# Kernel optimization log

Hardware: AMD Instinct MI355X
Metric: run time of the kernel (lower is better)

The kernel has to match this reference:

```python
import jax, jax.numpy as jnp
import numpy as np

B, S, D = 64, 500, 1024  # batch, seq_len, input_dim == hidden_dim
MAX_POS = 500

def _lin(k, din, dout):
    k1, k2 = jax.random.split(k)
    s = 1.0 / np.sqrt(din)
    W = jax.random.uniform(k1, (din, dout), jnp.float32, -s, s)
    b = jax.random.uniform(k2, (dout,), jnp.float32, -s, s)
    return W, b

def setup_inputs() -> dict:
    key = jax.random.key(0)
    ks = jax.random.split(key, 12)
    x = jax.random.normal(ks[0], (B, S, D), jnp.float32)
    pos_emb = jax.random.normal(ks[1], (MAX_POS, D), jnp.float32)
    Wq_fw, bq_fw = _lin(ks[2], D, D)
    Wk_fw, bk_fw = _lin(ks[3], D, D)
    Wv_fw, bv_fw = _lin(ks[4], D, D)
    Wq_bw, bq_bw = _lin(ks[5], D, D)
    Wk_bw, bk_bw = _lin(ks[6], D, D)
    Wv_bw, bv_bw = _lin(ks[7], D, D)
    Wg_fw, bg_fw = _lin(ks[8], 2 * D, D)
    Wg_bw, bg_bw = _lin(ks[9], 2 * D, D)
    W2, b2 = _lin(ks[10], 2 * D, 2 * D)
    W1, b1 = _lin(ks[11], 2 * D, 2 * D)
    return dict(x=x, pos_emb=pos_emb,
                Wq_fw=Wq_fw, bq_fw=bq_fw, Wk_fw=Wk_fw, bk_fw=bk_fw, Wv_fw=Wv_fw, bv_fw=bv_fw,
                Wq_bw=Wq_bw, bq_bw=bq_bw, Wk_bw=Wk_bw, bk_bw=bk_bw, Wv_bw=Wv_bw, bv_bw=bv_bw,
                Wg_fw=Wg_fw, bg_fw=bg_fw, Wg_bw=Wg_bw, bg_bw=bg_bw,
                W2=W2, b2=b2, W1=W1, b1=b1)

def _attn(q, k, v, mask, d):
    # q,k,v: [B,S,D]; mask: [S,S] bool (True = keep)
    scores = jnp.einsum('bqd,bkd->bqk', q, k) / jnp.sqrt(jnp.float32(d))
    scores = jnp.where(mask[None], scores, jnp.float32(-1e9))
    probs = jax.nn.softmax(scores, axis=-1)  # dropout is identity in eval
    return jnp.einsum('bqk,bkd->bqd', probs, v)

def reference(x, pos_emb, Wq_fw, bq_fw, Wk_fw, bk_fw, Wv_fw, bv_fw,
              Wq_bw, bq_bw, Wk_bw, bk_bw, Wv_bw, bv_bw,
              Wg_fw, bg_fw, Wg_bw, bg_bw, W2, b2, W1, b1):
    b, s, d = x.shape
    H = x + pos_emb[:s][None]  # [B,S,D]
    tri = jnp.tril(jnp.ones((s, s), dtype=bool))
    H_mF = _attn(H @ Wq_fw + bq_fw, H @ Wk_fw + bk_fw, H @ Wv_fw + bv_fw, tri, d)
    H_mB = _attn(H @ Wq_bw + bq_bw, H @ Wk_bw + bk_bw, H @ Wv_bw + bv_bw, tri.T, d)
    G_fw = jax.nn.sigmoid(jnp.concatenate([H, H_mF], -1) @ Wg_fw + bg_fw)
    C_F = G_fw * H + (1.0 - G_fw) * H_mF
    G_bw = jax.nn.sigmoid(jnp.concatenate([H, H_mB], -1) @ Wg_bw + bg_bw)
    C_B = G_bw * H + (1.0 - G_bw) * H_mB
    C_i = jnp.concatenate([C_F, C_B], -1)  # [B,S,2D]
    activ = jax.nn.sigmoid(C_i @ W2 + b2)
    scores = activ @ W1 + b1
    attn_w = jax.nn.softmax(scores, axis=1)  # softmax over seq dim
    utt_vec = jnp.sum(attn_w * C_i, axis=1)  # [B,2D]
    return utt_vec, C_i
```

## Files before the change

kernel.cpp:

```cpp
#include <hip/hip_runtime.h>

typedef __bf16 bf16;
typedef __bf16 bf16x4 __attribute__((ext_vector_type(4)));
typedef __bf16 bf16x8 __attribute__((ext_vector_type(8)));
typedef float  f32x4  __attribute__((ext_vector_type(4)));
typedef unsigned int u32;

#define GLD_LDS16(gsrc, ldst) \
  __builtin_amdgcn_global_load_lds((const __attribute__((address_space(1))) u32*)(gsrc), \
                                   (__attribute__((address_space(3))) u32*)(ldst), 16, 0, 0)

static __device__ __forceinline__ float sigmoidf_(float x) { return 1.0f / (1.0f + expf(-x)); }

__global__ void fill_guard(float* __restrict__ utt, float v) {
  int i = blockIdx.x * 256 + threadIdx.x;
  if (i < 131072) utt[i] = v;
}

__global__ void add_pos_bf(const float* __restrict__ x, const float* __restrict__ pos,
                           bf16* __restrict__ H) {
  size_t i = ((size_t)blockIdx.x * 256 + threadIdx.x) * 4;
  if (i >= 32768000ull) return;
  int d = (int)(i & 1023);
  int s = (int)((i >> 10) % 500);
  float4 xv = *(const float4*)(x + i);
  float4 pv = *(const float4*)(pos + (size_t)s * 1024 + d);
  bf16x4 o;
  o[0] = (bf16)(xv.x + pv.x); o[1] = (bf16)(xv.y + pv.y);
  o[2] = (bf16)(xv.z + pv.z); o[3] = (bf16)(xv.w + pv.w);
  *(bf16x4*)(H + i) = o;
}

__global__ void wtrans(const float* __restrict__ src, bf16* __restrict__ dst, int R, int C) {
  __shared__ float tile[32][33];
  int c0 = blockIdx.x * 32, r0 = blockIdx.y * 32;
  int tr = threadIdx.x >> 5, tc = threadIdx.x & 31;
#pragma unroll
  for (int i = 0; i < 4; ++i)
    tile[tr + i * 8][tc] = src[(size_t)(r0 + tr + i * 8) * C + c0 + tc];
  __syncthreads();
#pragma unroll
  for (int i = 0; i < 4; ++i) {
    int rr = tr + i * 8;
    dst[(size_t)(c0 + rr) * R + r0 + tc] = (bf16)tile[tc][rr];
  }
}

template <int EPI, typename TC>
__global__ __launch_bounds__(256, 2) void mgemm(
    const bf16* __restrict__ A, const bf16* __restrict__ A2, int ksplit,
    const bf16* __restrict__ Bt, const float* __restrict__ bias, TC* __restrict__ C,
    bf16* __restrict__ Cbf,
    int M, int N, int K, int lda, int ldb, int ldc, int c_off, float scale,
    long long sA, long long sB, long long sC,
    const bf16* __restrict__ Gh, const bf16* __restrict__ Gm) {
  __shared__ __align__(16) char sm[16384];
  const int t = threadIdx.x;
  const long long bz = blockIdx.z;
  A += bz * sA; A2 += bz * sA; Bt += bz * sB; C += bz * sC;

  const int gx = gridDim.x;
  const int nwg = gx * gridDim.y;
  const int orig = blockIdx.y * gx + blockIdx.x;
  const int qq = nwg >> 3, r8 = nwg & 7;
  const int xcd = orig & 7, lo = orig >> 3;
  const int wg = (xcd < r8 ? xcd * (qq + 1) : r8 * (qq + 1) + (xcd - r8) * qq) + lo;
  const int m0 = (wg / gx) * 128, n0 = (wg % gx) * 128;

  f32x4 acc[4][4];
#pragma unroll
  for (int i = 0; i < 4; ++i)
#pragma unroll
    for (int j = 0; j < 4; ++j)
#pragma unroll
      for (int c = 0; c < 4; ++c) acc[i][j][c] = 0.0f;

  const int lane = t & 63;
  const int wv = t >> 6, wm = (wv >> 1) * 64, wn = (wv & 1) * 64;
  const int lr = lane & 15, lkb = (lane >> 4) * 16;
  const int rr = t >> 2, cc = (t & 3) * 8;

  for (int k0 = 0; k0 < K; k0 += 32) {
    const bf16* Ak = (k0 < ksplit) ? (A + k0) : (A2 + (k0 - ksplit));
    const bf16* Bk = Bt + k0;
#pragma unroll
    for (int j = 0; j < 2; ++j) {
      int ra = m0 + j * 64 + rr; ra = ra < M ? ra : M - 1;
      GLD_LDS16(Ak + (size_t)ra * lda + cc, sm + j * 4096 + t * 16);
      int rb = n0 + j * 64 + rr; rb = rb < N ? rb : N - 1;
      GLD_LDS16(Bk + (size_t)rb * ldb + cc, sm + 8192 + j * 4096 + t * 16);
    }
    asm volatile("s_waitcnt vmcnt(0)" ::: "memory");
    __syncthreads();

    bf16x8 av[4], bv[4];
#pragma unroll
    for (int i = 0; i < 4; ++i) {
      av[i] = *(const bf16x8*)(sm + (wm + i * 16 + lr) * 64 + lkb);
      bv[i] = *(const bf16x8*)(sm + 8192 + (wn + i * 16 + lr) * 64 + lkb);
    }
#pragma unroll
    for (int i = 0; i < 4; ++i)
#pragma unroll
      for (int j = 0; j < 4; ++j)
        acc[i][j] = __builtin_amdgcn_mfma_f32_16x16x32_bf16(av[i], bv[j], acc[i][j], 0, 0, 0);
    __syncthreads();
  }

#pragma unroll
  for (int i = 0; i < 4; ++i) {
#pragma unroll
    for (int j4 = 0; j4 < 4; ++j4) {
      int m = m0 + wm + i * 16 + (lane >> 4) * 4 + j4;
      if (m >= M) continue;
#pragma unroll
      for (int j = 0; j < 4; ++j) {
        int n = n0 + wn + j * 16 + (lane & 15);
        if (n >= N) continue;
        float v = acc[i][j][j4] * scale;
        if (bias) v += bias[n];
        if (EPI == 1) v = sigmoidf_(v);
        if (EPI == 2) {
          float g = sigmoidf_(v);
          float h  = (float)Gh[(size_t)m * 1024 + n];
          float hm = (float)Gm[(size_t)m * 1024 + n];
          v = g * h + (1.0f - g) * hm;
        }
        if (EPI == 3) {
          unsigned b = (unsigned)m / 500u;
          unsigned s = (unsigned)m - b * 500u;
          C[(size_t)b * 524288 + (size_t)n * 512 + s] = (TC)v;
        } else {
          C[(size_t)m * ldc + c_off + n] = (TC)v;
          if (EPI == 2 && Cbf) Cbf[(size_t)m * 2048 + c_off + n] = (bf16)v;
        }
      }
    }
  }
}

__global__ void attn_softmax_w(const float* __restrict__ S, bf16* __restrict__ P, int fw) {
  int row = blockIdx.x * 4 + (threadIdx.x >> 6);
  int lane = threadIdx.x & 63;
  int q = row % 500;
  const float* Srow = S + (size_t)row * 512;
  bf16* Prow = P + (size_t)row * 512;
  int klo = fw ? 0 : q;
  int khi = fw ? q : 499;

  float xv[8];
  float m = -1e30f;
#pragma unroll
  for (int i = 0; i < 8; ++i) {
    int k = lane + i * 64;
    bool valid = (k >= klo) & (k <= khi);
    float v = valid ? Srow[k] : -1e30f;
    xv[i] = v;
    m = fmaxf(m, v);
  }
#pragma unroll
  for (int off = 32; off > 0; off >>= 1) m = fmaxf(m, __shfl_xor(m, off, 64));
  float e[8];
  float sum = 0.0f;
#pragma unroll
  for (int i = 0; i < 8; ++i) {
    e[i] = (xv[i] > -1e29f) ? expf(xv[i] - m) : 0.0f;
    sum += e[i];
  }
#pragma unroll
  for (int off = 32; off > 0; off >>= 1) sum += __shfl_xor(sum, off, 64);
  float inv = 1.0f / sum;
#pragma unroll
  for (int i = 0; i < 8; ++i) Prow[lane + i * 64] = (bf16)(e[i] * inv);
}

__global__ void final_reduce_chunk(const float* __restrict__ s2, const float* __restrict__ Ci,
                                   float* __restrict__ utt) {
  int c = blockIdx.x * 256 + threadIdx.x;
  int b = blockIdx.y;
  if (c >= 2048) return;
  float m = -1e30f, sum = 0.0f, acc = 0.0f;
  for (int s = 0; s < 500; ++s) {
    size_t idx = ((size_t)(b * 500 + s)) * 2048 + c;
    float xx = s2[idx];
    float ci = Ci[idx];
    float mn = fmaxf(m, xx);
    float corr = expf(m - mn);
    float e = expf(xx - mn);
    sum = sum * corr + e;
    acc = acc * corr + e * ci;
    m = mn;
  }
  utt[(size_t)b * 2048 + c] = acc / sum;
}

extern "C" void kernel_launch(void* const* d_in, const int* in_sizes, int n_in,
                              void* d_out, int out_size, void* d_ws, size_t ws_size,
                              hipStream_t stream) {
  (void)in_sizes; (void)n_in; (void)out_size;
  float* utt = (float*)d_out;
  float* Ci  = (float*)d_out + 131072;

  const float* x     = (const float*)d_in[0];
  const float* pos   = (const float*)d_in[1];
  const float* Wq_fw = (const float*)d_in[2];  const float* bq_fw = (const float*)d_in[3];
  const float* Wk_fw = (const float*)d_in[4];  const float* bk_fw = (const float*)d_in[5];
  const float* Wv_fw = (const float*)d_in[6];  const float* bv_fw = (const float*)d_in[7];
  const float* Wq_bw = (const float*)d_in[8];  const float* bq_bw = (const float*)d_in[9];
  const float* Wk_bw = (const float*)d_in[10]; const float* bk_bw = (const float*)d_in[11];
  const float* Wv_bw = (const float*)d_in[12]; const float* bv_bw = (const float*)d_in[13];
  const float* Wg_fw = (const float*)d_in[14]; const float* bg_fw = (const float*)d_in[15];
  const float* Wg_bw = (const float*)d_in[16]; const float* bg_bw = (const float*)d_in[17];
  const float* W2    = (const float*)d_in[18]; const float* b2    = (const float*)d_in[19];
  const float* W1    = (const float*)d_in[20]; const float* b1    = (const float*)d_in[21];

  const size_t WS_BYTES = 465305600ull;
  if (ws_size < WS_BYTES) { fill_guard<<<512, 256, 0, stream>>>(utt, 500.0f); return; }

  char* wsb = (char*)d_ws;
  bf16*  Hbf  = (bf16*)(wsb);
  bf16*  Qb   = (bf16*)(wsb + 65536000);
  bf16*  Kb   = (bf16*)(wsb + 131072000);
  bf16*  Vt   = (bf16*)(wsb + 196608000);
  float* Sb   = (float*)(wsb + 263716864);
  bf16*  Hmb  = (bf16*)(wsb + 263716864);
  bf16*  Pb   = (bf16*)(wsb + 329252864);
  char*  wts  = wsb + 362020864;
  bf16* WqF = (bf16*)(wts);             bf16* WkF = (bf16*)(wts + 2097152);
  bf16* WvF = (bf16*)(wts + 4194304);   bf16* WqB = (bf16*)(wts + 6291456);
  bf16* WkB = (bf16*)(wts + 8388608);   bf16* WvB = (bf16*)(wts + 10485760);
  bf16* WgF = (bf16*)(wts + 12582912);  bf16* WgB = (bf16*)(wts + 16777216);
  bf16* W2t = (bf16*)(wts + 20971520);  bf16* W1t = (bf16*)(wts + 29360128);
  bf16*  Cibf  = (bf16*)(wsb + 399769600);
  bf16*  activ = (bf16*)(wsb + 131072000);
  float* s2b   = (float*)(wsb);

  add_pos_bf<<<32000, 256, 0, stream>>>(x, pos, Hbf);

  struct WT { const float* s; bf16* d; int R, C; } wt[10] = {
      {Wq_fw, WqF, 1024, 1024}, {Wk_fw, WkF, 1024, 1024}, {Wv_fw, WvF, 1024, 1024},
      {Wq_bw, WqB, 1024, 1024}, {Wk_bw, WkB, 1024, 1024}, {Wv_bw, WvB, 1024, 1024},
      {Wg_fw, WgF, 2048, 1024}, {Wg_bw, WgB, 2048, 1024},
      {W2,    W2t, 2048, 2048}, {W1,    W1t, 2048, 2048}};
  for (int i = 0; i < 10; ++i)
    wtrans<<<dim3(wt[i].C / 32, wt[i].R / 32), 256, 0, stream>>>(wt[i].s, wt[i].d, wt[i].R, wt[i].C);

  const int BIG = 1 << 30;
  for (int dir = 0; dir < 2; ++dir) {
    const bf16* WqT = dir ? WqB : WqF;  const float* bq = dir ? bq_bw : bq_fw;
    const bf16* WkT = dir ? WkB : WkF;  const float* bk = dir ? bk_bw : bk_fw;
    const bf16* WvT = dir ? WvB : WvF;  const float* bv = dir ? bv_bw : bv_fw;
    const bf16* WgT = dir ? WgB : WgF;  const float* bg = dir ? bg_bw : bg_fw;

    mgemm<0, bf16><<<dim3(8, 250, 1), 256, 0, stream>>>(
        Hbf, Hbf, BIG, WqT, bq, Qb, nullptr, 32000, 1024, 1024, 1024, 1024, 1024, 0, 1.0f,
        0, 0, 0, nullptr, nullptr);
    mgemm<0, bf16><<<dim3(8, 250, 1), 256, 0, stream>>>(
        Hbf, Hbf, BIG, WkT, bk, Kb, nullptr, 32000, 1024, 1024, 1024, 1024, 1024, 0, 1.0f,
        0, 0, 0, nullptr, nullptr);
    mgemm<3, bf16><<<dim3(8, 250, 1), 256, 0, stream>>>(
        Hbf, Hbf, BIG, WvT, bv, Vt, nullptr, 32000, 1024, 1024, 1024, 1024, 512, 0, 1.0f,
        0, 0, 0, nullptr, nullptr);
    mgemm<0, float><<<dim3(4, 4, 64), 256, 0, stream>>>(
        Qb, Qb, BIG, Kb, nullptr, Sb, nullptr, 500, 500, 1024, 1024, 1024, 512, 0, 0.03125f,
        512000, 512000, 256000, nullptr, nullptr);
    attn_softmax_w<<<8000, 256, 0, stream>>>(Sb, Pb, dir == 0 ? 1 : 0);
    mgemm<0, bf16><<<dim3(8, 4, 64), 256, 0, stream>>>(
        Pb, Pb, BIG, Vt, nullptr, Hmb, nullptr, 500, 1024, 512, 512, 512, 1024, 0, 1.0f,
        256000, 524288, 512000, nullptr, nullptr);
    mgemm<2, float><<<dim3(8, 250, 1), 256, 0, stream>>>(
        Hbf, Hmb, 1024, WgT, bg, Ci, Cibf, 32000, 1024, 2048, 1024, 2048, 2048,
        dir == 0 ? 0 : 1024, 1.0f, 0, 0, 0, Hbf, Hmb);
  }

  mgemm<1, bf16><<<dim3(16, 250, 1), 256, 0, stream>>>(
      Cibf, Cibf, BIG, W2t, b2, activ, nullptr, 32000, 2048, 2048, 2048, 2048, 2048, 0, 1.0f,
      0, 0, 0, nullptr, nullptr);

  for (int c0 = 0; c0 < 2; ++c0) {
    mgemm<0, float><<<dim3(16, 125, 1), 256, 0, stream>>>(
        activ + (size_t)c0 * 16000 * 2048, activ, BIG, W1t, b1, s2b, nullptr,
        16000, 2048, 2048, 2048, 2048, 2048, 0, 1.0f, 0, 0, 0, nullptr, nullptr);
    final_reduce_chunk<<<dim3(8, 32), 256, 0, stream>>>(
        s2b, Ci + (size_t)c0 * 32 * 500 * 2048, utt + (size_t)c0 * 32 * 2048);
  }
}
```

Measured before the change: 2.610 ms.

## Add 256x256 double-buffered swizzled GEMM kernel for large projection GEMMs

Adds a new 512-thread GEMM kernel with 256x256 output tiles, K-step 64, double-buffered LDS (128KB dynamic shared memory) with XOR-swizzled layout, and prefetch of the next tile interleaved with MFMA phases using setprio. The large dense projections (Q/K/V, gates, W2, W1) switch to it, while the batched attention GEMMs keep the old 128x128 kernel, now stripped of the unused Cbf argument and XCD remapping. The aim is more data reuse per load and overlap of global loads with compute. The cost is much higher register and LDS use, which leaves only one block per CU.

```diff
diff --git a/kernel.cpp b/kernel.cpp
--- a/kernel.cpp
+++ b/kernel.cpp
@@ -47,17 +47,14 @@
 }
 
 template <int EPI, typename TC>
-__global__ __launch_bounds__(256, 2) void mgemm(
+__global__ __launch_bounds__(512, 2) void mgemm256(
     const bf16* __restrict__ A, const bf16* __restrict__ A2, int ksplit,
     const bf16* __restrict__ Bt, const float* __restrict__ bias, TC* __restrict__ C,
     bf16* __restrict__ Cbf,
     int M, int N, int K, int lda, int ldb, int ldc, int c_off, float scale,
-    long long sA, long long sB, long long sC,
     const bf16* __restrict__ Gh, const bf16* __restrict__ Gm) {
-  __shared__ __align__(16) char sm[16384];
+  extern __shared__ char sm[];
   const int t = threadIdx.x;
-  const long long bz = blockIdx.z;
-  A += bz * sA; A2 += bz * sA; Bt += bz * sB; C += bz * sC;
 
   const int gx = gridDim.x;
   const int nwg = gx * gridDim.y;
@@ -65,59 +62,107 @@
   const int qq = nwg >> 3, r8 = nwg & 7;
   const int xcd = orig & 7, lo = orig >> 3;
   const int wg = (xcd < r8 ? xcd * (qq + 1) : r8 * (qq + 1) + (xcd - r8) * qq) + lo;
-  const int m0 = (wg / gx) * 128, n0 = (wg % gx) * 128;
-
-  f32x4 acc[4][4];
-#pragma unroll
-  for (int i = 0; i < 4; ++i)
+  const int m0 = (wg / gx) * 256, n0 = (wg % gx) * 256;
+
+  const int lane = t & 63;
+  const int w = t >> 6, wr = w >> 2, wc = w & 3;
+  const int srow = t >> 3, schunk = t & 7, scol = schunk * 8;
+  const int hi16 = (lane >> 4) << 4;
+
+  f32x4 acc[8][4];
+#pragma unroll
+  for (int i = 0; i < 8; ++i)
 #pragma unroll
     for (int j = 0; j < 4; ++j)
 #pragma unroll
       for (int c = 0; c < 4; ++c) acc[i][j][c] = 0.0f;
 
-  const int lane = t & 63;
-  const int wv = t >> 6, wm = (wv >> 1) * 64, wn = (wv & 1) * 64;
-  const int lr = lane & 15, lkb = (lane >> 4) * 16;
-  const int rr = t >> 2, cc = (t & 3) * 8;
-
-  for (int k0 = 0; k0 < K; k0 += 32) {
-    const bf16* Ak = (k0 < ksplit) ? (A + k0) : (A2 + (k0 - ksplit));
-    const bf16* Bk = Bt + k0;
-#pragma unroll
-    for (int j = 0; j < 2; ++j) {
-      int ra = m0 + j * 64 + rr; ra = ra < M ? ra : M - 1;
-      GLD_LDS16(Ak + (size_t)ra * lda + cc, sm + j * 4096 + t * 16);
-      int rb = n0 + j * 64 + rr; rb = rb < N ? rb : N - 1;
-      GLD_LDS16(Bk + (size_t)rb * ldb + cc, sm + 8192 + j * 4096 + t * 16);
-    }
-    asm volatile("s_waitcnt vmcnt(0)" ::: "memory");
-    __syncthreads();
-
-    bf16x8 av[4], bv[4];
-#pragma unroll
-    for (int i = 0; i < 4; ++i) {
-      av[i] = *(const bf16x8*)(sm + (wm + i * 16 + lr) * 64 + lkb);
-      bv[i] = *(const bf16x8*)(sm + 8192 + (wn + i * 16 + lr) * 64 + lkb);
-    }
-#pragma unroll
-    for (int i = 0; i < 4; ++i)
-#pragma unroll
-      for (int j = 0; j < 4; ++j)
-        acc[i][j] = __builtin_amdgcn_mfma_f32_16x16x32_bf16(av[i], bv[j], acc[i][j], 0, 0, 0);
-    __syncthreads();
-  }
-
-#pragma unroll
-  for (int i = 0; i < 4; ++i) {
+#define STAGE_Q(tt, cb, h) do {                                                     \
+    const int k0s_ = (tt) * 64;                                                     \
+    char* lb_ = sm + (cb) * 65536 + ((h) < 2 ? 0 : 32768);                          \
+    _Pragma("unroll")                                                               \
+    for (int i_ = 0; i_ < 2; ++i_) {                                                \
+      int rl_ = ((h) & 1) * 128 + i_ * 64 + srow;                                   \
+      int cx_ = scol ^ ((rl_ & 7) << 3);                                            \
+      if ((h) < 2) {                                                                \
+        int rg_ = m0 + rl_; rg_ = rg_ < M ? rg_ : M - 1;                            \
+        const bf16* s_ = (k0s_ < ksplit)                                            \
+            ? A  + (size_t)rg_ * lda + k0s_ + cx_                                   \
+            : A2 + (size_t)rg_ * lda + (k0s_ - ksplit) + cx_;                       \
+        GLD_LDS16(s_, lb_ + rl_ * 128 + schunk * 16);                               \
+      } else {                                                                      \
+        int rg_ = n0 + rl_; rg_ = rg_ < N ? rg_ : N - 1;                            \
+        GLD_LDS16(Bt + (size_t)rg_ * ldb + k0s_ + cx_, lb_ + rl_ * 128 + schunk * 16); \
+      }                                                                             \
+    }                                                                               \
+  } while (0)
+
+  const int NT = K >> 6;
+  STAGE_Q(0, 0, 0); STAGE_Q(0, 0, 1); STAGE_Q(0, 0, 2); STAGE_Q(0, 0, 3);
+
+  for (int t0 = 0; t0 < NT; ++t0) {
+    const int cur = t0 & 1;
+    char* smA = sm + cur * 65536;
+    char* smB = smA + 32768;
+    const bool pf = (t0 + 1 < NT);
+
+    if (pf) {
+      STAGE_Q(t0 + 1, cur ^ 1, 0);
+      asm volatile("s_waitcnt vmcnt(2)" ::: "memory");
+    } else {
+      asm volatile("s_waitcnt vmcnt(0)" ::: "memory");
+    }
+    __builtin_amdgcn_s_barrier();
+
+    bf16x8 bfr[4][2];
+#pragma unroll
+    for (int fc = 0; fc < 4; ++fc)
+#pragma unroll
+      for (int ks = 0; ks < 2; ++ks) {
+        int rb = wc * 64 + fc * 16 + (lane & 15);
+        int byb = (ks * 64 + hi16) ^ ((rb & 7) << 4);
+        bfr[fc][ks] = *(const bf16x8*)(smB + rb * 128 + byb);
+      }
+
+#pragma unroll
+    for (int p = 0; p < 4; ++p) {
+      if (p > 0 && pf) STAGE_Q(t0 + 1, cur ^ 1, p);
+      bf16x8 afr[2][2];
+#pragma unroll
+      for (int e = 0; e < 2; ++e)
+#pragma unroll
+        for (int ks = 0; ks < 2; ++ks) {
+          int ra = wr * 128 + (2 * p + e) * 16 + (lane & 15);
+          int bya = (ks * 64 + hi16) ^ ((ra & 7) << 4);
+          afr[e][ks] = *(const bf16x8*)(smA + ra * 128 + bya);
+        }
+      if (p > 0) __builtin_amdgcn_s_barrier();
+      __builtin_amdgcn_s_setprio(1);
+#pragma unroll
+      for (int e = 0; e < 2; ++e)
+#pragma unroll
+        for (int fc = 0; fc < 4; ++fc)
+#pragma unroll
+          for (int ks = 0; ks < 2; ++ks)
+            acc[2 * p + e][fc] = __builtin_amdgcn_mfma_f32_16x16x32_bf16(
+                afr[e][ks], bfr[fc][ks], acc[2 * p + e][fc], 0, 0, 0);
+      __builtin_amdgcn_s_setprio(0);
+      __builtin_amdgcn_s_barrier();
+    }
+  }
+#undef STAGE_Q
+
+#pragma unroll
+  for (int fr = 0; fr < 8; ++fr) {
 #pragma unroll
     for (int j4 = 0; j4 < 4; ++j4) {
-      int m = m0 + wm + i * 16 + (lane >> 4) * 4 + j4;
+      int m = m0 + wr * 128 + fr * 16 + ((lane >> 4) << 2) + j4;
       if (m >= M) continue;
 #pragma unroll
-      for (int j = 0; j < 4; ++j) {
-        int n = n0 + wn + j * 16 + (lane & 15);
+      for (int fc = 0; fc < 4; ++fc) {
+        int n = n0 + wc * 64 + fc * 16 + (lane & 15);
         if (n >= N) continue;
-        float v = acc[i][j][j4] * scale;
+        float v = acc[fr][fc][j4] * scale;
         if (bias) v += bias[n];
         if (EPI == 1) v = sigmoidf_(v);
         if (EPI == 2) {
@@ -139,6 +184,77 @@
   }
 }
 
+template <int EPI, typename TC>
+__global__ __launch_bounds__(256, 2) void mgemm(
+    const bf16* __restrict__ A, const bf16* __restrict__ A2, int ksplit,
+    const bf16* __restrict__ Bt, const float* __restrict__ bias, TC* __restrict__ C,
+    int M, int N, int K, int lda, int ldb, int ldc, int c_off, float scale,
+    long long sA, long long sB, long long sC,
+    const bf16* __restrict__ Gh, const bf16* __restrict__ Gm) {
+  __shared__ __align__(16) char sm[16384];
+  const int t = threadIdx.x;
+  const long long bz = blockIdx.z;
+  A += bz * sA; A2 += bz * sA; Bt += bz * sB; C += bz * sC;
+  const int m0 = blockIdx.y * 128, n0 = blockIdx.x * 128;
+
+  f32x4 acc[4][4];
+#pragma unroll
+  for (int i = 0; i < 4; ++i)
+#pragma unroll
+    for (int j = 0; j < 4; ++j)
+#pragma unroll
+      for (int c = 0; c < 4; ++c) acc[i][j][c] = 0.0f;
+
+  const int lane = t & 63;
+  const int wv = t >> 6, wm = (wv >> 1) * 64, wn = (wv & 1) * 64;
+  const int lr = lane & 15, lkb = (lane >> 4) * 16;
+  const int rr = t >> 2, cc = (t & 3) * 8;
+
+  for (int k0 = 0; k0 < K; k0 += 32) {
+    const bf16* Ak = (k0 < ksplit) ? (A + k0) : (A2 + (k0 - ksplit));
+    const bf16* Bk = Bt + k0;
+#pragma unroll
+    for (int j = 0; j < 2; ++j) {
+      int ra = m0 + j * 64 + rr; ra = ra < M ? ra : M - 1;
+      GLD_LDS16(Ak + (size_t)ra * lda + cc, sm + j * 4096 + t * 16);
+      int rb = n0 + j * 64 + rr; rb = rb < N ? rb : N - 1;
+      GLD_LDS16(Bk + (size_t)rb * ldb + cc, sm + 8192 + j * 4096 + t * 16);
+    }
+    asm volatile("s_waitcnt vmcnt(0)" ::: "memory");
+    __syncthreads();
+
+    bf16x8 av[4], bv[4];
+#pragma unroll
+    for (int i = 0; i < 4; ++i) {
+      av[i] = *(const bf16x8*)(sm + (wm + i * 16 + lr) * 64 + lkb);
+      bv[i] = *(const bf16x8*)(sm + 8192 + (wn + i * 16 + lr) * 64 + lkb);
+    }
+#pragma unroll
+    for (int i = 0; i < 4; ++i)
+#pragma unroll
+      for (int j = 0; j < 4; ++j)
+        acc[i][j] = __builtin_amdgcn_mfma_f32_16x16x32_bf16(av[i], bv[j], acc[i][j], 0, 0, 0);
+    __syncthreads();
+  }
+
+#pragma unroll
+  for (int i = 0; i < 4; ++i) {
+#pragma unroll
+    for (int j4 = 0; j4 < 4; ++j4) {
+      int m = m0 + wm + i * 16 + (lane >> 4) * 4 + j4;
+      if (m >= M) continue;
+#pragma unroll
+      for (int j = 0; j < 4; ++j) {
+        int n = n0 + wn + j * 16 + (lane & 15);
+        if (n >= N) continue;
+        float v = acc[i][j][j4] * scale;
+        if (bias) v += bias[n];
+        C[(size_t)m * ldc + c_off + n] = (TC)v;
+      }
+    }
+  }
+}
+
 __global__ void attn_softmax_w(const float* __restrict__ S, bf16* __restrict__ P, int fw) {
   int row = blockIdx.x * 4 + (threadIdx.x >> 6);
   int lane = threadIdx.x & 63;
@@ -235,6 +351,17 @@
   bf16*  activ = (bf16*)(wsb + 131072000);
   float* s2b   = (float*)(wsb);
 
+  hipFuncSetAttribute(reinterpret_cast<const void*>(&mgemm256<0, bf16>),
+                      hipFuncAttributeMaxDynamicSharedMemorySize, 131072);
+  hipFuncSetAttribute(reinterpret_cast<const void*>(&mgemm256<3, bf16>),
+                      hipFuncAttributeMaxDynamicSharedMemorySize, 131072);
+  hipFuncSetAttribute(reinterpret_cast<const void*>(&mgemm256<2, float>),
+                      hipFuncAttributeMaxDynamicSharedMemorySize, 131072);
+  hipFuncSetAttribute(reinterpret_cast<const void*>(&mgemm256<1, bf16>),
+                      hipFuncAttributeMaxDynamicSharedMemorySize, 131072);
+  hipFuncSetAttribute(reinterpret_cast<const void*>(&mgemm256<0, float>),
+                      hipFuncAttributeMaxDynamicSharedMemorySize, 131072);
+
   add_pos_bf<<<32000, 256, 0, stream>>>(x, pos, Hbf);
 
   struct WT { const float* s; bf16* d; int R, C; } wt[10] = {
@@ -252,35 +379,35 @@
     const bf16* WvT = dir ? WvB : WvF;  const float* bv = dir ? bv_bw : bv_fw;
     const bf16* WgT = dir ? WgB : WgF;  const float* bg = dir ? bg_bw : bg_fw;
 
-    mgemm<0, bf16><<<dim3(8, 250, 1), 256, 0, stream>>>(
+    mgemm256<0, bf16><<<dim3(4, 125), 512, 131072, stream>>>(
         Hbf, Hbf, BIG, WqT, bq, Qb, nullptr, 32000, 1024, 1024, 1024, 1024, 1024, 0, 1.0f,
-        0, 0, 0, nullptr, nullptr);
-    mgemm<0, bf16><<<dim3(8, 250, 1), 256, 0, stream>>>(
+        nullptr, nullptr);
+    mgemm256<0, bf16><<<dim3(4, 125), 512, 131072, stream>>>(
         Hbf, Hbf, BIG, WkT, bk, Kb, nullptr, 32000, 1024, 1024, 1024, 1024, 1024, 0, 1.0f,
-        0, 0, 0, nullptr, nullptr);
-    mgemm<3, bf16><<<dim3(8, 250, 1), 256, 0, stream>>>(
+        nullptr, nullptr);
+    mgemm256<3, bf16><<<dim3(4, 125), 512, 131072, stream>>>(
         Hbf, Hbf, BIG, WvT, bv, Vt, nullptr, 32000, 1024, 1024, 1024, 1024, 512, 0, 1.0f,
-        0, 0, 0, nullptr, nullptr);
+        nullptr, nullptr);
     mgemm<0, float><<<dim3(4, 4, 64), 256, 0, stream>>>(
-        Qb, Qb, BIG, Kb, nullptr, Sb, nullptr, 500, 500, 1024, 1024, 1024, 512, 0, 0.03125f,
+        Qb, Qb, BIG, Kb, nullptr, Sb, 500, 500, 1024, 1024, 1024, 512, 0, 0.03125f,
         512000, 512000, 256000, nullptr, nullptr);
     attn_softmax_w<<<8000, 256, 0, stream>>>(Sb, Pb, dir == 0 ? 1 : 0);
     mgemm<0, bf16><<<dim3(8, 4, 64), 256, 0, stream>>>(
-        Pb, Pb, BIG, Vt, nullptr, Hmb, nullptr, 500, 1024, 512, 512, 512, 1024, 0, 1.0f,
+        Pb, Pb, BIG, Vt, nullptr, Hmb, 500, 1024, 512, 512, 512, 1024, 0, 1.0f,
         256000, 524288, 512000, nullptr, nullptr);
-    mgemm<2, float><<<dim3(8, 250, 1), 256, 0, stream>>>(
+    mgemm256<2, float><<<dim3(8, 125), 512, 131072, stream>>>(
         Hbf, Hmb, 1024, WgT, bg, Ci, Cibf, 32000, 1024, 2048, 1024, 2048, 2048,
-        dir == 0 ? 0 : 1024, 1.0f, 0, 0, 0, Hbf, Hmb);
-  }
-
-  mgemm<1, bf16><<<dim3(16, 250, 1), 256, 0, stream>>>(
+        dir == 0 ? 0 : 1024, 1.0f, Hbf, Hmb);
+  }
+
+  mgemm256<1, bf16><<<dim3(8, 125), 512, 131072, stream>>>(
       Cibf, Cibf, BIG, W2t, b2, activ, nullptr, 32000, 2048, 2048, 2048, 2048, 2048, 0, 1.0f,
-      0, 0, 0, nullptr, nullptr);
+      nullptr, nullptr);
 
   for (int c0 = 0; c0 < 2; ++c0) {
-    mgemm<0, float><<<dim3(16, 125, 1), 256, 0, stream>>>(
+    mgemm256<0, float><<<dim3(8, 63), 512, 131072, stream>>>(
         activ + (size_t)c0 * 16000 * 2048, activ, BIG, W1t, b1, s2b, nullptr,
-        16000, 2048, 2048, 2048, 2048, 2048, 0, 1.0f, 0, 0, 0, nullptr, nullptr);
+        16000, 2048, 2048, 2048, 2048, 2048, 0, 1.0f, nullptr, nullptr);
     final_reduce_chunk<<<dim3(8, 32), 256, 0, stream>>>(
         s2b, Ci + (size_t)c0 * 32 * 500 * 2048, utt + (size_t)c0 * 32 * 2048);
   }
```

Result: slower. 2.856 ms (+9.4%).

## Fuse QKV projections into one GEMM and use K=64 tiles with XOR-swizzled LDS

Applied to the files above, without the earlier changes.

The Q, K and V projections now run as a single GEMM with N=3072 over the contiguous transposed weights. A new epilogue routes each column range to Q, K or the transposed V layout, each with its own bias. The GEMM main loop now stages 64-wide K slices into a 32KB LDS buffer with an XOR swizzle, to halve barrier and loop overhead and to avoid LDS bank conflicts. The larger LDS footprint may lower occupancy, and the fused epilogue adds branching.

```diff
diff --git a/kernel.cpp b/kernel.cpp
--- a/kernel.cpp
+++ b/kernel.cpp
@@ -49,12 +49,13 @@
 template <int EPI, typename TC>
 __global__ __launch_bounds__(256, 2) void mgemm(
     const bf16* __restrict__ A, const bf16* __restrict__ A2, int ksplit,
-    const bf16* __restrict__ Bt, const float* __restrict__ bias, TC* __restrict__ C,
-    bf16* __restrict__ Cbf,
+    const bf16* __restrict__ Bt, const float* __restrict__ bias,
+    const float* __restrict__ biasK, const float* __restrict__ biasV,
+    TC* __restrict__ C, bf16* __restrict__ Cbf, bf16* __restrict__ Cv,
     int M, int N, int K, int lda, int ldb, int ldc, int c_off, float scale,
     long long sA, long long sB, long long sC,
     const bf16* __restrict__ Gh, const bf16* __restrict__ Gm) {
-  __shared__ __align__(16) char sm[16384];
+  __shared__ __align__(16) char sm[32768];
   const int t = threadIdx.x;
   const long long bz = blockIdx.z;
   A += bz * sA; A2 += bz * sA; Bt += bz * sB; C += bz * sC;
@@ -77,33 +78,44 @@
 
   const int lane = t & 63;
   const int wv = t >> 6, wm = (wv >> 1) * 64, wn = (wv & 1) * 64;
-  const int lr = lane & 15, lkb = (lane >> 4) * 16;
-  const int rr = t >> 2, cc = (t & 3) * 8;
-
-  for (int k0 = 0; k0 < K; k0 += 32) {
+  const int lr = lane & 15, lhi = lane >> 4;
+  const int srow8 = t >> 3, sch = t & 7;
+
+  for (int k0 = 0; k0 < K; k0 += 64) {
     const bf16* Ak = (k0 < ksplit) ? (A + k0) : (A2 + (k0 - ksplit));
     const bf16* Bk = Bt + k0;
 #pragma unroll
-    for (int j = 0; j < 2; ++j) {
-      int ra = m0 + j * 64 + rr; ra = ra < M ? ra : M - 1;
-      GLD_LDS16(Ak + (size_t)ra * lda + cc, sm + j * 4096 + t * 16);
-      int rb = n0 + j * 64 + rr; rb = rb < N ? rb : N - 1;
-      GLD_LDS16(Bk + (size_t)rb * ldb + cc, sm + 8192 + j * 4096 + t * 16);
+    for (int i = 0; i < 4; ++i) {
+      int rl = i * 32 + srow8;
+      int ra = m0 + rl; ra = ra < M ? ra : M - 1;
+      int ca = (sch ^ (ra & 7)) * 8;
+      GLD_LDS16(Ak + (size_t)ra * lda + ca, sm + rl * 128 + sch * 16);
+      int rb = n0 + rl; rb = rb < N ? rb : N - 1;
+      int cb = (sch ^ (rb & 7)) * 8;
+      GLD_LDS16(Bk + (size_t)rb * ldb + cb, sm + 16384 + rl * 128 + sch * 16);
     }
     asm volatile("s_waitcnt vmcnt(0)" ::: "memory");
     __syncthreads();
 
-    bf16x8 av[4], bv[4];
-#pragma unroll
-    for (int i = 0; i < 4; ++i) {
-      av[i] = *(const bf16x8*)(sm + (wm + i * 16 + lr) * 64 + lkb);
-      bv[i] = *(const bf16x8*)(sm + 8192 + (wn + i * 16 + lr) * 64 + lkb);
-    }
+    bf16x8 av[4][2], bv[4][2];
 #pragma unroll
     for (int i = 0; i < 4; ++i)
 #pragma unroll
-      for (int j = 0; j < 4; ++j)
-        acc[i][j] = __builtin_amdgcn_mfma_f32_16x16x32_bf16(av[i], bv[j], acc[i][j], 0, 0, 0);
+      for (int ks = 0; ks < 2; ++ks) {
+        int ra = wm + i * 16 + lr;
+        int ga = ks * 4 + lhi;
+        av[i][ks] = *(const bf16x8*)(sm + ra * 128 + ((ga ^ (ra & 7)) << 4));
+        int rb = wn + i * 16 + lr;
+        bv[i][ks] = *(const bf16x8*)(sm + 16384 + rb * 128 + ((ga ^ (rb & 7)) << 4));
+      }
+#pragma unroll
+    for (int ks = 0; ks < 2; ++ks)
+#pragma unroll
+      for (int i = 0; i < 4; ++i)
+#pragma unroll
+        for (int j = 0; j < 4; ++j)
+          acc[i][j] = __builtin_amdgcn_mfma_f32_16x16x32_bf16(av[i][ks], bv[j][ks],
+                                                              acc[i][j], 0, 0, 0);
     __syncthreads();
   }
 
@@ -111,13 +123,23 @@
   for (int i = 0; i < 4; ++i) {
 #pragma unroll
     for (int j4 = 0; j4 < 4; ++j4) {
-      int m = m0 + wm + i * 16 + (lane >> 4) * 4 + j4;
+      int m = m0 + wm + i * 16 + lhi * 4 + j4;
       if (m >= M) continue;
 #pragma unroll
       for (int j = 0; j < 4; ++j) {
-        int n = n0 + wn + j * 16 + (lane & 15);
+        int n = n0 + wn + j * 16 + lr;
         if (n >= N) continue;
         float v = acc[i][j][j4] * scale;
+        if (EPI == 4) {
+          const float* bp = (n < 1024) ? bias : (n < 2048) ? biasK : biasV;
+          v += bp[n & 1023];
+          unsigned b = (unsigned)m / 500u;
+          unsigned s = (unsigned)m - b * 500u;
+          if (n < 1024)       C  [(size_t)m * 1024 + n] = (TC)v;
+          else if (n < 2048)  Cbf[(size_t)m * 1024 + (n - 1024)] = (bf16)v;
+          else                Cv [(size_t)b * 524288 + (size_t)(n - 2048) * 512 + s] = (bf16)v;
+          continue;
+        }
         if (bias) v += bias[n];
         if (EPI == 1) v = sigmoidf_(v);
         if (EPI == 2) {
@@ -126,14 +148,8 @@
           float hm = (float)Gm[(size_t)m * 1024 + n];
           v = g * h + (1.0f - g) * hm;
         }
-        if (EPI == 3) {
-          unsigned b = (unsigned)m / 500u;
-          unsigned s = (unsigned)m - b * 500u;
-          C[(size_t)b * 524288 + (size_t)n * 512 + s] = (TC)v;
-        } else {
-          C[(size_t)m * ldc + c_off + n] = (TC)v;
-          if (EPI == 2 && Cbf) Cbf[(size_t)m * 2048 + c_off + n] = (bf16)v;
-        }
+        C[(size_t)m * ldc + c_off + n] = (TC)v;
+        if (EPI == 2 && Cbf) Cbf[(size_t)m * 2048 + c_off + n] = (bf16)v;
       }
     }
   }
@@ -226,9 +242,8 @@
   bf16*  Hmb  = (bf16*)(wsb + 263716864);
   bf16*  Pb   = (bf16*)(wsb + 329252864);
   char*  wts  = wsb + 362020864;
-  bf16* WqF = (bf16*)(wts);             bf16* WkF = (bf16*)(wts + 2097152);
-  bf16* WvF = (bf16*)(wts + 4194304);   bf16* WqB = (bf16*)(wts + 6291456);
-  bf16* WkB = (bf16*)(wts + 8388608);   bf16* WvB = (bf16*)(wts + 10485760);
+  bf16* WqF = (bf16*)(wts);
+  bf16* WqB = (bf16*)(wts + 6291456);
   bf16* WgF = (bf16*)(wts + 12582912);  bf16* WgB = (bf16*)(wts + 16777216);
   bf16* W2t = (bf16*)(wts + 20971520);  bf16* W1t = (bf16*)(wts + 29360128);
   bf16*  Cibf  = (bf16*)(wsb + 399769600);
@@ -238,8 +253,9 @@
   add_pos_bf<<<32000, 256, 0, stream>>>(x, pos, Hbf);
 
   struct WT { const float* s; bf16* d; int R, C; } wt[10] = {
-      {Wq_fw, WqF, 1024, 1024}, {Wk_fw, WkF, 1024, 1024}, {Wv_fw, WvF, 1024, 1024},
-      {Wq_bw, WqB, 1024, 1024}, {Wk_bw, WkB, 1024, 1024}, {Wv_bw, WvB, 1024, 1024},
+      {Wq_fw, WqF, 1024, 1024}, {Wk_fw, (bf16*)(wts + 2097152), 1024, 1024},
+      {Wv_fw, (bf16*)(wts + 4194304), 1024, 1024}, {Wq_bw, WqB, 1024, 1024},
+      {Wk_bw, (bf16*)(wts + 8388608), 1024, 1024}, {Wv_bw, (bf16*)(wts + 10485760), 1024, 1024},
       {Wg_fw, WgF, 2048, 1024}, {Wg_bw, WgB, 2048, 1024},
       {W2,    W2t, 2048, 2048}, {W1,    W1t, 2048, 2048}};
   for (int i = 0; i < 10; ++i)
@@ -247,40 +263,40 @@
 
   const int BIG = 1 << 30;
   for (int dir = 0; dir < 2; ++dir) {
-    const bf16* WqT = dir ? WqB : WqF;  const float* bq = dir ? bq_bw : bq_fw;
-    const bf16* WkT = dir ? WkB : WkF;  const float* bk = dir ? bk_bw : bk_fw;
-    const bf16* WvT = dir ? WvB : WvF;  const float* bv = dir ? bv_bw : bv_fw;
-    const bf16* WgT = dir ? WgB : WgF;  const float* bg = dir ? bg_bw : bg_fw;
-
-    mgemm<0, bf16><<<dim3(8, 250, 1), 256, 0, stream>>>(
-        Hbf, Hbf, BIG, WqT, bq, Qb, nullptr, 32000, 1024, 1024, 1024, 1024, 1024, 0, 1.0f,
-        0, 0, 0, nullptr, nullptr);
-    mgemm<0, bf16><<<dim3(8, 250, 1), 256, 0, stream>>>(
-        Hbf, Hbf, BIG, WkT, bk, Kb, nullptr, 32000, 1024, 1024, 1024, 1024, 1024, 0, 1.0f,
-        0, 0, 0, nullptr, nullptr);
-    mgemm<3, bf16><<<dim3(8, 250, 1), 256, 0, stream>>>(
-        Hbf, Hbf, BIG, WvT, bv, Vt, nullptr, 32000, 1024, 1024, 1024, 1024, 512, 0, 1.0f,
-        0, 0, 0, nullptr, nullptr);
+    const bf16* WqkvT = dir ? WqB : WqF;
+    const bf16* WgT = dir ? WgB : WgF;
+    const float* bq = dir ? bq_bw : bq_fw;
+    const float* bk = dir ? bk_bw : bk_fw;
+    const float* bv = dir ? bv_bw : bv_fw;
+    const float* bg = dir ? bg_bw : bg_fw;
+
+    mgemm<4, bf16><<<dim3(24, 250, 1), 256, 0, stream>>>(
+        Hbf, Hbf, BIG, WqkvT, bq, bk, bv, Qb, Kb, Vt,
+        32000, 3072, 1024, 1024, 1024, 1024, 0, 1.0f, 0, 0, 0, nullptr, nullptr);
     mgemm<0, float><<<dim3(4, 4, 64), 256, 0, stream>>>(
-        Qb, Qb, BIG, Kb, nullptr, Sb, nullptr, 500, 500, 1024, 1024, 1024, 512, 0, 0.03125f,
-        512000, 512000, 256000, nullptr, nullptr);
+        Qb, Qb, BIG, Kb, nullptr, nullptr, nullptr, Sb, nullptr, nullptr,
+        500, 500, 1024, 1024, 1024, 512, 0, 0.03125f, 512000, 512000, 256000,
+        nullptr, nullptr);
     attn_softmax_w<<<8000, 256, 0, stream>>>(Sb, Pb, dir == 0 ? 1 : 0);
     mgemm<0, bf16><<<dim3(8, 4, 64), 256, 0, stream>>>(
-        Pb, Pb, BIG, Vt, nullptr, Hmb, nullptr, 500, 1024, 512, 512, 512, 1024, 0, 1.0f,
-        256000, 524288, 512000, nullptr, nullptr);
+        Pb, Pb, BIG, Vt, nullptr, nullptr, nullptr, Hmb, nullptr, nullptr,
+        500, 1024, 512, 512, 512, 1024, 0, 1.0f, 256000, 524288, 512000,
+        nullptr, nullptr);
     mgemm<2, float><<<dim3(8, 250, 1), 256, 0, stream>>>(
-        Hbf, Hmb, 1024, WgT, bg, Ci, Cibf, 32000, 1024, 2048, 1024, 2048, 2048,
-        dir == 0 ? 0 : 1024, 1.0f, 0, 0, 0, Hbf, Hmb);
+        Hbf, Hmb, 1024, WgT, bg, nullptr, nullptr, Ci, Cibf, nullptr,
+        32000, 1024, 2048, 1024, 2048, 2048, dir == 0 ? 0 : 1024, 1.0f, 0, 0, 0,
+        Hbf, Hmb);
   }
 
   mgemm<1, bf16><<<dim3(16, 250, 1), 256, 0, stream>>>(
-      Cibf, Cibf, BIG, W2t, b2, activ, nullptr, 32000, 2048, 2048, 2048, 2048, 2048, 0, 1.0f,
-      0, 0, 0, nullptr, nullptr);
+      Cibf, Cibf, BIG, W2t, b2, nullptr, nullptr, activ, nullptr, nullptr,
+      32000, 2048, 2048, 2048, 2048, 2048, 0, 1.0f, 0, 0, 0, nullptr, nullptr);
 
   for (int c0 = 0; c0 < 2; ++c0) {
     mgemm<0, float><<<dim3(16, 125, 1), 256, 0, stream>>>(
-        activ + (size_t)c0 * 16000 * 2048, activ, BIG, W1t, b1, s2b, nullptr,
-        16000, 2048, 2048, 2048, 2048, 2048, 0, 1.0f, 0, 0, 0, nullptr, nullptr);
+        activ + (size_t)c0 * 16000 * 2048, activ, BIG, W1t, b1, nullptr, nullptr,
+        s2b, nullptr, nullptr, 16000, 2048, 2048, 2048, 2048, 2048, 0, 1.0f,
+        0, 0, 0, nullptr, nullptr);
     final_reduce_chunk<<<dim3(8, 32), 256, 0, stream>>>(
         s2b, Ci + (size_t)c0 * 32 * 500 * 2048, utt + (size_t)c0 * 32 * 2048);
   }
```

Measured after the change: 2.401 ms. 8.0% less time.
